# Kernel optimization log

Measured on AMD Instinct MI355X. Metric: run time of the kernel, lower is better.

## Reference

```python
import jax, jax.numpy as jnp
import numpy as np

B = 1; IMG = 256; P = 16; INC = 3; C = 384; NH = 12; HD = C // NH
WS = 8; SH = WS // 2; HP = IMG // P; L = HP * HP; NW = (HP // WS) ** 2
NB = 12; OC = 4; EPS = 1e-5; MLP = 4 * C


def _rel_index(w):
    coords = np.stack(np.meshgrid(np.arange(w), np.arange(w), indexing='ij'))
    cf = coords.reshape(2, -1)
    rel = (cf[:, :, None] - cf[:, None, :]).transpose(1, 2, 0)
    rel[:, :, 0] += w - 1
    rel[:, :, 1] += w - 1
    rel[:, :, 0] *= 2 * w - 1
    return rel.sum(-1)  # (w*w, w*w)


def _attn_mask():
    m = np.zeros((HP, HP))
    cnt = 0
    for hs in (slice(0, -WS), slice(-WS, -SH), slice(-SH, None)):
        for ws_ in (slice(0, -WS), slice(-WS, -SH), slice(-SH, None)):
            m[hs, ws_] = cnt
            cnt += 1
    mw = m.reshape(HP // WS, WS, HP // WS, WS).transpose(0, 2, 1, 3).reshape(-1, WS * WS)
    d = mw[:, None, :] - mw[:, :, None]
    return np.where(d != 0, -100.0, 0.0).astype(np.float32)  # (NW, 64, 64)

_REL_IDX = jnp.asarray(_rel_index(WS))
_AMASK = jnp.asarray(_attn_mask())


def _ln(x, w, b):
    m = jnp.mean(x, -1, keepdims=True)
    d = x - m
    v = jnp.mean(d * d, -1, keepdims=True)
    return d * jax.lax.rsqrt(v + EPS) * w + b


def _resize_ac(x, oh, ow):
    # bilinear, align_corners=True
    H, W = x.shape[-2], x.shape[-1]
    def idx(o, n):
        s = jnp.linspace(0.0, n - 1.0, o)
        i0 = jnp.floor(s).astype(jnp.int32)
        i1 = jnp.minimum(i0 + 1, n - 1)
        return i0, i1, (s - i0.astype(s.dtype)).astype(x.dtype)
    y0, y1, wy = idx(oh, H)
    x0, x1, wx = idx(ow, W)
    r = x[..., y0, :] * (1 - wy)[:, None] + x[..., y1, :] * wy[:, None]
    return r[..., x0] * (1 - wx) + r[..., x1] * wx


def setup_inputs():
    key = jax.random.key(0)
    ks = jax.random.split(key, 16)
    f32 = jnp.float32
    def rn(k, shape, s=0.02):
        return jax.random.normal(k, shape, dtype=f32) * s
    return {
        'x': jax.random.normal(ks[0], (B, INC, IMG, IMG), f32),
        'patch_w': rn(ks[1], (C, INC, P, P), 0.05),
        'patch_b': jnp.zeros((C,), f32),
        'pos_embed': rn(ks[2], (1, L, C)),
        'ln1_w': jnp.ones((NB, C), f32), 'ln1_b': jnp.zeros((NB, C), f32),
        'qkv_w': rn(ks[3], (NB, 3 * C, C)),
        'proj_w': rn(ks[4], (NB, C, C)), 'proj_b': jnp.zeros((NB, C), f32),
        'rpb': rn(ks[5], (NB, (2 * WS - 1) ** 2, NH)),
        'ln2_w': jnp.ones((NB, C), f32), 'ln2_b': jnp.zeros((NB, C), f32),
        'fc1_w': rn(ks[6], (NB, MLP, C)), 'fc1_b': jnp.zeros((NB, MLP), f32),
        'fc2_w': rn(ks[7], (NB, C, MLP)), 'fc2_b': jnp.zeros((NB, C), f32),
        'skip_w': rn(ks[8], (OC, C), 0.05), 'skip_b': jnp.zeros((OC,), f32),
        'dt1_w': rn(ks[9], (C, INC, P, P), 0.05), 'dt1_b': jnp.zeros((INC,), f32),
        'bn1_w': jnp.ones((INC,), f32), 'bn1_b': jnp.zeros((INC,), f32),
        'dt2_w': rn(ks[10], (INC, OC, P, P), 0.05), 'dt2_b': jnp.zeros((OC,), f32),
        'bn2_w': jnp.ones((OC,), f32), 'bn2_b': jnp.zeros((OC,), f32),
    }


def reference(x, patch_w, patch_b, pos_embed, ln1_w, ln1_b, qkv_w, proj_w, proj_b,
              rpb, ln2_w, ln2_b, fc1_w, fc1_b, fc2_w, fc2_b, skip_w, skip_b,
              dt1_w, dt1_b, bn1_w, bn1_b, dt2_w, dt2_b, bn2_w, bn2_b):
    scale = HD ** -0.5
    # --- patch embed (conv k=P, s=P) ---
    xr = x.reshape(B, INC, HP, P, HP, P)
    f = jnp.einsum('bchpwq,ocpq->bohw', xr, patch_w) + patch_b[None, :, None, None]
    # --- buggy token flatten, replicated exactly from the source ---
    t = jnp.transpose(f.reshape(B, C, P, HP // P, P, HP // P), (0, 3, 5, 1, 2, 4)).reshape(B, L, C)
    t = t + pos_embed

    def block(h, p):
        l1w, l1b, qw, pw, pb, rt, l2w, l2b, f1w, f1b, f2w, f2b = p
        sc = h
        y = _ln(h, l1w, l1b).reshape(B, HP, HP, C)
        y = jnp.roll(y, (-SH, -SH), axis=(1, 2))  # every block is shifted in this model
        yw = y.reshape(B, HP // WS, WS, HP // WS, WS, C).transpose(0, 1, 3, 2, 4, 5)
        yw = yw.reshape(B * NW, WS * WS, C)
        qkv = (yw @ qw.T).reshape(B * NW, WS * WS, 3, NH, HD).transpose(2, 0, 3, 1, 4)
        q, k, v = qkv[0], qkv[1], qkv[2]
        attn = jnp.einsum('wnid,wnjd->wnij', q, k) * scale
        bias = rt[_REL_IDX].transpose(2, 0, 1)  # (NH, 64, 64)
        attn = attn + bias[None]
        attn = attn.reshape(B, NW, NH, WS * WS, WS * WS) + _AMASK[None, :, None]
        attn = jax.nn.softmax(attn.reshape(B * NW, NH, WS * WS, WS * WS), axis=-1)
        o = jnp.einsum('wnij,wnjd->wnid', attn, v).transpose(0, 2, 1, 3).reshape(B * NW, WS * WS, C)
        o = o @ pw.T + pb
        o = o.reshape(B, HP // WS, HP // WS, WS, WS, C).transpose(0, 1, 3, 2, 4, 5).reshape(B, HP, HP, C)
        o = jnp.roll(o, (SH, SH), axis=(1, 2)).reshape(B, L, C)
        h = sc + o
        z = _ln(h, l2w, l2b)
        z = jax.nn.gelu(z @ f1w.T + f1b, approximate=False)
        h = h + (z @ f2w.T + f2b)
        return h, None

    t, _ = jax.lax.scan(block, t, (ln1_w, ln1_b, qkv_w, proj_w, proj_b, rpb,
                                   ln2_w, ln2_b, fc1_w, fc1_b, fc2_w, fc2_b))

    f = t.reshape(B, HP, HP, C).transpose(0, 3, 1, 2)  # (B, C, 16, 16)
    # --- decoder ---
    skip = jnp.einsum('bchw,oc->bohw', f, skip_w) + skip_b[None, :, None, None]
    # interpolate(skip, size=(H, W)) with H, W == skip's own size: identity.
    d = jnp.einsum('bchw,cokl->bohkwl', f, dt1_w).reshape(B, INC, HP * P, HP * P) + dt1_b[None, :, None, None]
    d = jax.nn.relu(d / jnp.sqrt(1.0 + EPS) * bn1_w[None, :, None, None] + bn1_b[None, :, None, None])
    d = jnp.einsum('bchw,cokl->bohkwl', d, dt2_w).reshape(B, OC, HP * P * P, HP * P * P) + dt2_b[None, :, None, None]
    d = d / jnp.sqrt(1.0 + EPS) * bn2_w[None, :, None, None] + bn2_b[None, :, None, None]
    # Upsample(scale_factor = IMG // (P*P) = 1): identity.
    skip_up = _resize_ac(skip, d.shape[2], d.shape[3])
    out = (d + skip_up).reshape(B, -1, IMG, IMG)
    return out
```

## Files before the change

kernel.cpp:

```cpp
#include <hip/hip_runtime.h>
#include <cmath>

typedef _Float16 v8h __attribute__((ext_vector_type(8)));
typedef float v4f __attribute__((ext_vector_type(4)));

#define DEV __device__ __forceinline__

DEV int win_map(int m) {
  int w = m >> 6, tok = m & 63;
  int r = ((w >> 1) * 8 + (tok >> 3) + 4) & 15;
  int c = ((w & 1) * 8 + (tok & 7) + 4) & 15;
  return r * 16 + c;
}

template<int MAP>
DEV float4 loadA4(const float* __restrict__ A, int m, int k, int K) {
  if constexpr (MAP == 0) {
    return *(const float4*)(A + (size_t)m * K + k);
  } else if constexpr (MAP == 1) {
    return *(const float4*)(A + (size_t)win_map(m) * 384 + k);
  } else {
    int h = m >> 4, w = m & 15;
    int inc = k >> 8, rem = k & 255, p = rem >> 4, q = rem & 15;
    return *(const float4*)(A + inc * 65536 + (h * 16 + p) * 256 + w * 16 + q);
  }
}

template<int WAVES_M, int WAVES_N, int WN, int MAP, bool LN, int EPI>
__launch_bounds__(256)
__global__ void mgemm(const float* __restrict__ A, const float* __restrict__ W,
                      const float* __restrict__ bias,
                      const float* __restrict__ lnw, const float* __restrict__ lnb,
                      const float* __restrict__ resid, const float* __restrict__ aux,
                      float* __restrict__ Cout, int N, int K) {
  constexpr int BM = WAVES_M * 16;
  constexpr int BN = WAVES_N * WN * 16;
  constexpr int BK = 64;
  constexpr int BKP = BK + 8;

  __shared__ _Float16 As[BM][BKP];
  __shared__ _Float16 Ws[BN][BKP];
  __shared__ float redS[256], redQ[256];
  __shared__ float lmean[BM], lrstd[BM];

  const int t = threadIdx.x;
  const int wave = t >> 6, lane = t & 63;
  const int m0 = blockIdx.y * BM, n0 = blockIdx.x * BN;

  if constexpr (LN) {
    constexpr int PARTS = 256 / BM;
    int r = t / PARTS, part = t % PARTS;
    int chunk = K / PARTS;
    float s = 0.f, sq = 0.f;
    for (int k = part * chunk; k < (part + 1) * chunk; k += 4) {
      float4 v = loadA4<MAP>(A, m0 + r, k, K);
      s += v.x + v.y + v.z + v.w;
      sq += v.x * v.x + v.y * v.y + v.z * v.z + v.w * v.w;
    }
    redS[t] = s; redQ[t] = sq;
    __syncthreads();
    if (t < BM) {
      float ss = 0.f, qq = 0.f;
      for (int p = 0; p < PARTS; ++p) { ss += redS[t * PARTS + p]; qq += redQ[t * PARTS + p]; }
      float mean = ss / K;
      float var = qq / K - mean * mean;
      lmean[t] = mean;
      lrstd[t] = rsqrtf(var + 1e-5f);
    }
    __syncthreads();
  }

  const int wm = wave % WAVES_M;
  const int wn = wave / WAVES_M;
  const int mBase = wm * 16;
  const int nBase = wn * (WN * 16);

  v4f acc[WN] = {};

  for (int k0 = 0; k0 < K; k0 += BK) {
    constexpr int AREP = (BM * 16) / 256;
#pragma unroll
    for (int i = 0; i < AREP; ++i) {
      int idx = t + i * 256;
      int row = idx >> 4;
      int kc = (idx & 15) * 4;
      float4 v = loadA4<MAP>(A, m0 + row, k0 + kc, K);
      if constexpr (LN) {
        float4 lw = *(const float4*)(lnw + k0 + kc);
        float4 lb = *(const float4*)(lnb + k0 + kc);
        float mu = lmean[row], rs = lrstd[row];
        v.x = (v.x - mu) * rs * lw.x + lb.x;
        v.y = (v.y - mu) * rs * lw.y + lb.y;
        v.z = (v.z - mu) * rs * lw.z + lb.z;
        v.w = (v.w - mu) * rs * lw.w + lb.w;
      }
      _Float16* dst = &As[row][kc];
      dst[0] = (_Float16)v.x; dst[1] = (_Float16)v.y;
      dst[2] = (_Float16)v.z; dst[3] = (_Float16)v.w;
    }
    constexpr int WREP = (BN * 16) / 256;
#pragma unroll
    for (int i = 0; i < WREP; ++i) {
      int idx = t + i * 256;
      int row = idx >> 4;
      int kc = (idx & 15) * 4;
      float4 v = *(const float4*)(W + (size_t)(n0 + row) * K + k0 + kc);
      _Float16* dst = &Ws[row][kc];
      dst[0] = (_Float16)v.x; dst[1] = (_Float16)v.y;
      dst[2] = (_Float16)v.z; dst[3] = (_Float16)v.w;
    }
    __syncthreads();
#pragma unroll
    for (int kk = 0; kk < BK; kk += 32) {
      v8h af = *(const v8h*)&As[mBase + (lane & 15)][kk + (lane >> 4) * 8];
#pragma unroll
      for (int nt = 0; nt < WN; ++nt) {
        v8h bf = *(const v8h*)&Ws[nBase + nt * 16 + (lane & 15)][kk + (lane >> 4) * 8];
        acc[nt] = __builtin_amdgcn_mfma_f32_16x16x32_f16(af, bf, acc[nt], 0, 0, 0);
      }
    }
    __syncthreads();
  }

  const int quad = lane >> 4;
  const int col = lane & 15;
#pragma unroll
  for (int nt = 0; nt < WN; ++nt) {
    int n = n0 + nBase + nt * 16 + col;
#pragma unroll
    for (int r = 0; r < 4; ++r) {
      int m = m0 + mBase + quad * 4 + r;
      float v = acc[nt][r];
      if constexpr (EPI == 0) {
        Cout[(size_t)m * N + n] = v;
      } else if constexpr (EPI == 1) {
        Cout[(size_t)m * N + n] = resid[(size_t)m * N + n] + v + bias[n];
      } else if constexpr (EPI == 2) {
        float z = v + bias[n];
        Cout[(size_t)m * N + n] = 0.5f * z * (1.0f + erff(z * 0.70710678118654752f));
      } else {
        Cout[n * 256 + m] = v + bias[n] + aux[n * 256 + m];
      }
    }
  }
}

__launch_bounds__(256)
__global__ void attn_k(const float* __restrict__ qkv, const float* __restrict__ rpb,
                       float* __restrict__ obuf) {
  __shared__ float qs[64][33], ks[64][33], vs[64][33];
  __shared__ float ps[64][68];
  __shared__ float rbias[225];
  __shared__ int labv[64];
  const int t = threadIdx.x;
  const int w = blockIdx.x & 3, head = blockIdx.x >> 2;

  for (int idx = t; idx < 2048; idx += 256) {
    int tok = idx >> 5, d = idx & 31;
    int base = (w * 64 + tok) * 1152 + head * 32 + d;
    qs[tok][d] = qkv[base];
    ks[tok][d] = qkv[base + 384];
    vs[tok][d] = qkv[base + 768];
  }
  for (int idx = t; idx < 225; idx += 256) rbias[idx] = rpb[idx * 12 + head];
  if (t < 64) {
    int r = (w >> 1) * 8 + (t >> 3), c = (w & 1) * 8 + (t & 7);
    int lr = r < 8 ? 0 : (r < 12 ? 1 : 2);
    int lc = c < 8 ? 0 : (c < 12 ? 1 : 2);
    labv[t] = lr * 3 + lc;
  }
  __syncthreads();

  const int tx = t & 15, ty = t >> 4;
  float acc[4][4] = {};
  for (int d = 0; d < 32; ++d) {
    float a[4], b[4];
#pragma unroll
    for (int ii = 0; ii < 4; ++ii) a[ii] = qs[ty * 4 + ii][d];
#pragma unroll
    for (int jj = 0; jj < 4; ++jj) b[jj] = ks[tx * 4 + jj][d];
#pragma unroll
    for (int ii = 0; ii < 4; ++ii)
#pragma unroll
      for (int jj = 0; jj < 4; ++jj) acc[ii][jj] += a[ii] * b[jj];
  }
  const float scale = 0.17677669529663687f;
#pragma unroll
  for (int ii = 0; ii < 4; ++ii) {
    int i = ty * 4 + ii;
    int yi = i >> 3, xi = i & 7, li = labv[i];
    float pv[4];
    float mx = -1e30f;
#pragma unroll
    for (int jj = 0; jj < 4; ++jj) {
      int j = tx * 4 + jj;
      int yj = j >> 3, xj = j & 7;
      int ri = (yi - yj + 7) * 15 + (xi - xj + 7);
      float s = acc[ii][jj] * scale + rbias[ri] + (li == labv[j] ? 0.f : -100.f);
      pv[jj] = s;
      mx = fmaxf(mx, s);
    }
    for (int off = 1; off < 16; off <<= 1) mx = fmaxf(mx, __shfl_xor(mx, off));
    float sum = 0.f;
#pragma unroll
    for (int jj = 0; jj < 4; ++jj) { pv[jj] = expf(pv[jj] - mx); sum += pv[jj]; }
    for (int off = 1; off < 16; off <<= 1) sum += __shfl_xor(sum, off);
    float inv = 1.0f / sum;
#pragma unroll
    for (int jj = 0; jj < 4; ++jj) ps[i][tx * 4 + jj] = pv[jj] * inv;
  }
  __syncthreads();

  float o2[4][2] = {};
  for (int j = 0; j < 64; ++j) {
    float v0 = vs[j][tx * 2 + 0], v1 = vs[j][tx * 2 + 1];
#pragma unroll
    for (int ii = 0; ii < 4; ++ii) {
      float p = ps[ty * 4 + ii][j];
      o2[ii][0] += p * v0;
      o2[ii][1] += p * v1;
    }
  }
#pragma unroll
  for (int ii = 0; ii < 4; ++ii) {
    int l = win_map(w * 64 + ty * 4 + ii);
    obuf[l * 384 + head * 32 + tx * 2 + 0] = o2[ii][0];
    obuf[l * 384 + head * 32 + tx * 2 + 1] = o2[ii][1];
  }
}

__global__ void skip_k(const float* __restrict__ hfin, const float* __restrict__ sw,
                       const float* __restrict__ sb, float* __restrict__ skipb) {
  int o = blockIdx.x, t = threadIdx.x;
  float acc = 0.f;
  for (int c = 0; c < 384; ++c) acc += hfin[t * 384 + c] * sw[o * 384 + c];
  skipb[o * 256 + t] = acc + sb[o];
}

__global__ void d1_k(const float* __restrict__ hfin, const float* __restrict__ wgt,
                     const float* __restrict__ bvec, const float* __restrict__ bnw,
                     const float* __restrict__ bnb, float* __restrict__ d1) {
  __shared__ float hs[2][384];
  const int t = threadIdx.x;
  const int l0 = blockIdx.x * 2;
  for (int idx = t; idx < 768; idx += 256) {
    int pi = idx / 384, c = idx % 384;
    hs[pi][c] = hfin[(l0 + pi) * 384 + c];
  }
  __syncthreads();
  const float invs = rsqrtf(1.0f + 1e-5f);
  const int kk = t >> 4, ll = t & 15;
  for (int o = 0; o < 3; ++o) {
    float a0 = 0.f, a1 = 0.f;
    for (int c = 0; c < 384; ++c) {
      float wv = wgt[c * 768 + o * 256 + t];
      a0 += hs[0][c] * wv;
      a1 += hs[1][c] * wv;
    }
    float sw = bnw[o] * invs, bb = bvec[o], sb = bnb[o];
    float v0 = fmaxf((a0 + bb) * sw + sb, 0.f);
    float v1 = fmaxf((a1 + bb) * sw + sb, 0.f);
#pragma unroll
    for (int pi = 0; pi < 2; ++pi) {
      int l = l0 + pi;
      int h = l >> 4, wq = l & 15;
      float v = pi ? v1 : v0;
      d1[o * 65536 + (h * 16 + kk) * 256 + (wq * 16 + ll)] = v;
    }
  }
}

__launch_bounds__(256)
__global__ void d2_k(const float* __restrict__ d1, const float* __restrict__ w2,
                     const float* __restrict__ b2, const float* __restrict__ bnw,
                     const float* __restrict__ bnb, const float* __restrict__ skipb,
                     float* __restrict__ out) {
  __shared__ float d1s[3][256];
  __shared__ float wcol[3][16];
  __shared__ float srow[16];
  const int t = threadIdx.x;
  const int y = blockIdx.x, o = blockIdx.y;
  const int h2 = y >> 4, k = y & 15;
  for (int idx = t; idx < 768; idx += 256) {
    int c = idx >> 8, wi = idx & 255;
    d1s[c][wi] = d1[c * 65536 + h2 * 256 + wi];
  }
  if (t < 48) {
    int c = t >> 4, l2 = t & 15;
    wcol[c][l2] = w2[c * 1024 + o * 256 + k * 16 + l2];
  }
  if (t < 16) {
    const float dy = 15.0f / 4095.0f;
    float s = y * dy;
    int y0 = min((int)s, 15);
    int y1 = min(y0 + 1, 15);
    float wy = s - (float)y0;
    float a0 = skipb[o * 256 + y0 * 16 + t];
    float a1 = skipb[o * 256 + y1 * 16 + t];
    srow[t] = a0 + (a1 - a0) * wy;
  }
  __syncthreads();
  const float invs = rsqrtf(1.0f + 1e-5f);
  const float sw = bnw[o] * invs;
  const float base = b2[o] * sw + bnb[o];
  const float dx = 15.0f / 4095.0f;
  const size_t obase = ((size_t)o << 24) + ((size_t)y << 12);
#pragma unroll
  for (int rep = 0; rep < 4; ++rep) {
    int x4 = t + rep * 256;
    int x = x4 * 4;
    int wi = x >> 4;
    int l2b = x & 15;
    float vals[4];
#pragma unroll
    for (int e = 0; e < 4; ++e) {
      int l2 = l2b + e;
      float v = d1s[0][wi] * wcol[0][l2] + d1s[1][wi] * wcol[1][l2] + d1s[2][wi] * wcol[2][l2];
      v = v * sw + base;
      float s = (float)(x + e) * dx;
      int x0 = min((int)s, 15);
      int x1 = min(x0 + 1, 15);
      float wx = s - (float)x0;
      vals[e] = v + srow[x0] + (srow[x1] - srow[x0]) * wx;
    }
    *(float4*)&out[obase + x] = make_float4(vals[0], vals[1], vals[2], vals[3]);
  }
}

extern "C" void kernel_launch(void* const* d_in, const int* in_sizes, int n_in,
                              void* d_out, int out_size, void* d_ws, size_t ws_size,
                              hipStream_t stream) {
  const float* x       = (const float*)d_in[0];
  const float* patch_w = (const float*)d_in[1];
  const float* patch_b = (const float*)d_in[2];
  const float* pos     = (const float*)d_in[3];
  const float* ln1w    = (const float*)d_in[4];
  const float* ln1b    = (const float*)d_in[5];
  const float* qkvw    = (const float*)d_in[6];
  const float* projw   = (const float*)d_in[7];
  const float* projb   = (const float*)d_in[8];
  const float* rpb     = (const float*)d_in[9];
  const float* ln2w    = (const float*)d_in[10];
  const float* ln2b    = (const float*)d_in[11];
  const float* fc1w    = (const float*)d_in[12];
  const float* fc1b    = (const float*)d_in[13];
  const float* fc2w    = (const float*)d_in[14];
  const float* fc2b    = (const float*)d_in[15];
  const float* skipw   = (const float*)d_in[16];
  const float* skipbi  = (const float*)d_in[17];
  const float* dt1w    = (const float*)d_in[18];
  const float* dt1b    = (const float*)d_in[19];
  const float* bn1w    = (const float*)d_in[20];
  const float* bn1b    = (const float*)d_in[21];
  const float* dt2w    = (const float*)d_in[22];
  const float* dt2b    = (const float*)d_in[23];
  const float* bn2w    = (const float*)d_in[24];
  const float* bn2b    = (const float*)d_in[25];
  float* out = (float*)d_out;
  float* ws = (float*)d_ws;

  float* h    = ws;
  float* qkvb = ws + 98304;
  float* obuf = ws + 393216;
  float* zb   = ws + 491520;
  float* d1b  = ws + 884736;
  float* skb  = ws + 1081344;

  mgemm<2, 2, 2, 2, false, 3><<<dim3(6, 8), 256, 0, stream>>>(
      x, patch_w, patch_b, nullptr, nullptr, nullptr, pos, h, 384, 768);

  for (int b = 0; b < 12; ++b) {
    mgemm<2, 2, 2, 1, true, 0><<<dim3(18, 8), 256, 0, stream>>>(
        h, qkvw + (size_t)b * 442368, nullptr, ln1w + b * 384, ln1b + b * 384,
        nullptr, nullptr, qkvb, 1152, 384);
    attn_k<<<48, 256, 0, stream>>>(qkvb, rpb + b * 2700, obuf);
    mgemm<1, 4, 1, 0, false, 1><<<dim3(6, 16), 256, 0, stream>>>(
        obuf, projw + (size_t)b * 147456, projb + b * 384, nullptr, nullptr,
        h, nullptr, h, 384, 384);
    mgemm<2, 2, 2, 0, true, 2><<<dim3(24, 8), 256, 0, stream>>>(
        h, fc1w + (size_t)b * 589824, fc1b + b * 1536, ln2w + b * 384, ln2b + b * 384,
        nullptr, nullptr, zb, 1536, 384);
    mgemm<1, 4, 1, 0, false, 1><<<dim3(6, 16), 256, 0, stream>>>(
        zb, fc2w + (size_t)b * 589824, fc2b + b * 384, nullptr, nullptr,
        h, nullptr, h, 384, 1536);
  }

  skip_k<<<4, 256, 0, stream>>>(h, skipw, skipbi, skb);
  d1_k<<<128, 256, 0, stream>>>(h, dt1w, dt1b, bn1w, bn1b, d1b);
  d2_k<<<dim3(4096, 4), 256, 0, stream>>>(d1b, dt2w, dt2b, bn2w, bn2b, skb, out);
}
```

Baseline: 1.408 ms.

## Fuse encoder launches into persistent megakernel with software grid barriers

```diff
diff --git a/kernel.cpp b/kernel.cpp
--- a/kernel.cpp
+++ b/kernel.cpp
@@ -5,6 +5,8 @@
 typedef float v4f __attribute__((ext_vector_type(4)));
 
 #define DEV __device__ __forceinline__
+
+constexpr int GRID = 256;
 
 DEV int win_map(int m) {
   int w = m >> 6, tok = m & 63;
@@ -26,26 +28,48 @@
   }
 }
 
+union SMem {
+  struct {
+    _Float16 As[32][72];
+    _Float16 Ws[64][72];
+    float redS[256], redQ[256];
+    float lmean[32], lrstd[32];
+  } g;
+  struct {
+    float qs[64][33], ks[64][33], vs[64][33];
+    float ps[64][68];
+    float rbias[225];
+    int lab[64];
+  } a;
+  struct {
+    float hs[2][384];
+  } d;
+};
+
+DEV void gsync(unsigned* cnt, unsigned& bar, int t) {
+  __threadfence();
+  __syncthreads();
+  bar += GRID;
+  if (t == 0) {
+    __hip_atomic_fetch_add(cnt, 1u, __ATOMIC_RELEASE, __HIP_MEMORY_SCOPE_AGENT);
+    while (__hip_atomic_load(cnt, __ATOMIC_RELAXED, __HIP_MEMORY_SCOPE_AGENT) < bar)
+      __builtin_amdgcn_s_sleep(1);
+    (void)__hip_atomic_load(cnt, __ATOMIC_ACQUIRE, __HIP_MEMORY_SCOPE_AGENT);
+  }
+  __syncthreads();
+}
+
 template<int WAVES_M, int WAVES_N, int WN, int MAP, bool LN, int EPI>
-__launch_bounds__(256)
-__global__ void mgemm(const float* __restrict__ A, const float* __restrict__ W,
-                      const float* __restrict__ bias,
-                      const float* __restrict__ lnw, const float* __restrict__ lnb,
-                      const float* __restrict__ resid, const float* __restrict__ aux,
-                      float* __restrict__ Cout, int N, int K) {
+DEV void gemm_tile(SMem& sm, const int t, const int m0, const int n0,
+                   const float* __restrict__ A, const float* __restrict__ W,
+                   const float* __restrict__ bias,
+                   const float* __restrict__ lnw, const float* __restrict__ lnb,
+                   const float* __restrict__ resid, const float* __restrict__ aux,
+                   float* __restrict__ Cout, int N, int K) {
   constexpr int BM = WAVES_M * 16;
   constexpr int BN = WAVES_N * WN * 16;
   constexpr int BK = 64;
-  constexpr int BKP = BK + 8;
-
-  __shared__ _Float16 As[BM][BKP];
-  __shared__ _Float16 Ws[BN][BKP];
-  __shared__ float redS[256], redQ[256];
-  __shared__ float lmean[BM], lrstd[BM];
-
-  const int t = threadIdx.x;
   const int wave = t >> 6, lane = t & 63;
-  const int m0 = blockIdx.y * BM, n0 = blockIdx.x * BN;
 
   if constexpr (LN) {
     constexpr int PARTS = 256 / BM;
@@ -57,15 +81,15 @@
       s += v.x + v.y + v.z + v.w;
       sq += v.x * v.x + v.y * v.y + v.z * v.z + v.w * v.w;
     }
-    redS[t] = s; redQ[t] = sq;
+    sm.g.redS[t] = s; sm.g.redQ[t] = sq;
     __syncthreads();
     if (t < BM) {
       float ss = 0.f, qq = 0.f;
-      for (int p = 0; p < PARTS; ++p) { ss += redS[t * PARTS + p]; qq += redQ[t * PARTS + p]; }
+      for (int p = 0; p < PARTS; ++p) { ss += sm.g.redS[t * PARTS + p]; qq += sm.g.redQ[t * PARTS + p]; }
       float mean = ss / K;
       float var = qq / K - mean * mean;
-      lmean[t] = mean;
-      lrstd[t] = rsqrtf(var + 1e-5f);
+      sm.g.lmean[t] = mean;
+      sm.g.lrstd[t] = rsqrtf(var + 1e-5f);
     }
     __syncthreads();
   }
@@ -88,13 +112,13 @@
       if constexpr (LN) {
         float4 lw = *(const float4*)(lnw + k0 + kc);
         float4 lb = *(const float4*)(lnb + k0 + kc);
-        float mu = lmean[row], rs = lrstd[row];
+        float mu = sm.g.lmean[row], rs = sm.g.lrstd[row];
         v.x = (v.x - mu) * rs * lw.x + lb.x;
         v.y = (v.y - mu) * rs * lw.y + lb.y;
         v.z = (v.z - mu) * rs * lw.z + lb.z;
         v.w = (v.w - mu) * rs * lw.w + lb.w;
       }
-      _Float16* dst = &As[row][kc];
+      _Float16* dst = &sm.g.As[row][kc];
       dst[0] = (_Float16)v.x; dst[1] = (_Float16)v.y;
       dst[2] = (_Float16)v.z; dst[3] = (_Float16)v.w;
     }
@@ -105,17 +129,17 @@
       int row = idx >> 4;
       int kc = (idx & 15) * 4;
       float4 v = *(const float4*)(W + (size_t)(n0 + row) * K + k0 + kc);
-      _Float16* dst = &Ws[row][kc];
+      _Float16* dst = &sm.g.Ws[row][kc];
       dst[0] = (_Float16)v.x; dst[1] = (_Float16)v.y;
       dst[2] = (_Float16)v.z; dst[3] = (_Float16)v.w;
     }
     __syncthreads();
 #pragma unroll
     for (int kk = 0; kk < BK; kk += 32) {
-      v8h af = *(const v8h*)&As[mBase + (lane & 15)][kk + (lane >> 4) * 8];
+      v8h af = *(const v8h*)&sm.g.As[mBase + (lane & 15)][kk + (lane >> 4) * 8];
 #pragma unroll
       for (int nt = 0; nt < WN; ++nt) {
-        v8h bf = *(const v8h*)&Ws[nBase + nt * 16 + (lane & 15)][kk + (lane >> 4) * 8];
+        v8h bf = *(const v8h*)&sm.g.Ws[nBase + nt * 16 + (lane & 15)][kk + (lane >> 4) * 8];
         acc[nt] = __builtin_amdgcn_mfma_f32_16x16x32_f16(af, bf, acc[nt], 0, 0, 0);
       }
     }
@@ -145,29 +169,24 @@
   }
 }
 
-__launch_bounds__(256)
-__global__ void attn_k(const float* __restrict__ qkv, const float* __restrict__ rpb,
-                       float* __restrict__ obuf) {
-  __shared__ float qs[64][33], ks[64][33], vs[64][33];
-  __shared__ float ps[64][68];
-  __shared__ float rbias[225];
-  __shared__ int labv[64];
-  const int t = threadIdx.x;
-  const int w = blockIdx.x & 3, head = blockIdx.x >> 2;
+DEV void attn_tile(SMem& sm, const int t, const int bid,
+                   const float* __restrict__ qkv, const float* __restrict__ rpb,
+                   float* __restrict__ obuf) {
+  const int w = bid & 3, head = bid >> 2;
 
   for (int idx = t; idx < 2048; idx += 256) {
     int tok = idx >> 5, d = idx & 31;
     int base = (w * 64 + tok) * 1152 + head * 32 + d;
-    qs[tok][d] = qkv[base];
-    ks[tok][d] = qkv[base + 384];
-    vs[tok][d] = qkv[base + 768];
-  }
-  for (int idx = t; idx < 225; idx += 256) rbias[idx] = rpb[idx * 12 + head];
+    sm.a.qs[tok][d] = qkv[base];
+    sm.a.ks[tok][d] = qkv[base + 384];
+    sm.a.vs[tok][d] = qkv[base + 768];
+  }
+  for (int idx = t; idx < 225; idx += 256) sm.a.rbias[idx] = rpb[idx * 12 + head];
   if (t < 64) {
     int r = (w >> 1) * 8 + (t >> 3), c = (w & 1) * 8 + (t & 7);
     int lr = r < 8 ? 0 : (r < 12 ? 1 : 2);
     int lc = c < 8 ? 0 : (c < 12 ? 1 : 2);
-    labv[t] = lr * 3 + lc;
+    sm.a.lab[t] = lr * 3 + lc;
   }
   __syncthreads();
 
@@ -176,9 +195,9 @@
   for (int d = 0; d < 32; ++d) {
     float a[4], b[4];
 #pragma unroll
-    for (int ii = 0; ii < 4; ++ii) a[ii] = qs[ty * 4 + ii][d];
-#pragma unroll
-    for (int jj = 0; jj < 4; ++jj) b[jj] = ks[tx * 4 + jj][d];
+    for (int ii = 0; ii < 4; ++ii) a[ii] = sm.a.qs[ty * 4 + ii][d];
+#pragma unroll
+    for (int jj = 0; jj < 4; ++jj) b[jj] = sm.a.ks[tx * 4 + jj][d];
 #pragma unroll
     for (int ii = 0; ii < 4; ++ii)
 #pragma unroll
@@ -188,7 +207,7 @@
 #pragma unroll
   for (int ii = 0; ii < 4; ++ii) {
     int i = ty * 4 + ii;
-    int yi = i >> 3, xi = i & 7, li = labv[i];
+    int yi = i >> 3, xi = i & 7, li = sm.a.lab[i];
     float pv[4];
     float mx = -1e30f;
 #pragma unroll
@@ -196,7 +215,7 @@
       int j = tx * 4 + jj;
       int yj = j >> 3, xj = j & 7;
       int ri = (yi - yj + 7) * 15 + (xi - xj + 7);
-      float s = acc[ii][jj] * scale + rbias[ri] + (li == labv[j] ? 0.f : -100.f);
+      float s = acc[ii][jj] * scale + sm.a.rbias[ri] + (li == sm.a.lab[j] ? 0.f : -100.f);
       pv[jj] = s;
       mx = fmaxf(mx, s);
     }
@@ -207,16 +226,16 @@
     for (int off = 1; off < 16; off <<= 1) sum += __shfl_xor(sum, off);
     float inv = 1.0f / sum;
 #pragma unroll
-    for (int jj = 0; jj < 4; ++jj) ps[i][tx * 4 + jj] = pv[jj] * inv;
+    for (int jj = 0; jj < 4; ++jj) sm.a.ps[i][tx * 4 + jj] = pv[jj] * inv;
   }
   __syncthreads();
 
   float o2[4][2] = {};
   for (int j = 0; j < 64; ++j) {
-    float v0 = vs[j][tx * 2 + 0], v1 = vs[j][tx * 2 + 1];
+    float v0 = sm.a.vs[j][tx * 2 + 0], v1 = sm.a.vs[j][tx * 2 + 1];
 #pragma unroll
     for (int ii = 0; ii < 4; ++ii) {
-      float p = ps[ty * 4 + ii][j];
+      float p = sm.a.ps[ty * 4 + ii][j];
       o2[ii][0] += p * v0;
       o2[ii][1] += p * v1;
     }
@@ -229,23 +248,14 @@
   }
 }
 
-__global__ void skip_k(const float* __restrict__ hfin, const float* __restrict__ sw,
-                       const float* __restrict__ sb, float* __restrict__ skipb) {
-  int o = blockIdx.x, t = threadIdx.x;
-  float acc = 0.f;
-  for (int c = 0; c < 384; ++c) acc += hfin[t * 384 + c] * sw[o * 384 + c];
-  skipb[o * 256 + t] = acc + sb[o];
-}
-
-__global__ void d1_k(const float* __restrict__ hfin, const float* __restrict__ wgt,
-                     const float* __restrict__ bvec, const float* __restrict__ bnw,
-                     const float* __restrict__ bnb, float* __restrict__ d1) {
-  __shared__ float hs[2][384];
-  const int t = threadIdx.x;
-  const int l0 = blockIdx.x * 2;
+DEV void d1_tile(SMem& sm, const int t, const int bid,
+                 const float* __restrict__ hfin, const float* __restrict__ wgt,
+                 const float* __restrict__ bvec, const float* __restrict__ bnw,
+                 const float* __restrict__ bnb, float* __restrict__ d1) {
+  const int l0 = bid * 2;
   for (int idx = t; idx < 768; idx += 256) {
     int pi = idx / 384, c = idx % 384;
-    hs[pi][c] = hfin[(l0 + pi) * 384 + c];
+    sm.d.hs[pi][c] = hfin[(l0 + pi) * 384 + c];
   }
   __syncthreads();
   const float invs = rsqrtf(1.0f + 1e-5f);
@@ -254,8 +264,8 @@
     float a0 = 0.f, a1 = 0.f;
     for (int c = 0; c < 384; ++c) {
       float wv = wgt[c * 768 + o * 256 + t];
-      a0 += hs[0][c] * wv;
-      a1 += hs[1][c] * wv;
+      a0 += sm.d.hs[0][c] * wv;
+      a1 += sm.d.hs[1][c] * wv;
     }
     float sw = bnw[o] * invs, bb = bvec[o], sb = bnb[o];
     float v0 = fmaxf((a0 + bb) * sw + sb, 0.f);
@@ -268,6 +278,78 @@
       d1[o * 65536 + (h * 16 + kk) * 256 + (wq * 16 + ll)] = v;
     }
   }
+}
+
+DEV void skip_tile(const int t, const int o,
+                   const float* __restrict__ hfin, const float* __restrict__ sw,
+                   const float* __restrict__ sb, float* __restrict__ skipb) {
+  float acc = 0.f;
+  for (int c = 0; c < 384; ++c) acc += hfin[t * 384 + c] * sw[o * 384 + c];
+  skipb[o * 256 + t] = acc + sb[o];
+}
+
+struct Params {
+  const float *x, *patch_w, *patch_b, *pos;
+  const float *ln1w, *ln1b, *qkvw, *projw, *projb, *rpb, *ln2w, *ln2b;
+  const float *fc1w, *fc1b, *fc2w, *fc2b;
+  const float *skipw, *skipbi, *dt1w, *dt1b, *bn1w, *bn1b;
+  float *h, *qkvb, *obuf, *zb, *d1b, *skb;
+  unsigned* cnt;
+};
+
+__launch_bounds__(256)
+__global__ void mega_k(Params p) {
+  __shared__ SMem sm;
+  const int t = threadIdx.x;
+  const int bid = blockIdx.x;
+  unsigned bar = 0;
+
+  if (bid < 48) {
+    gemm_tile<2, 2, 2, 2, false, 3>(sm, t, (bid / 6) * 32, (bid % 6) * 64,
+        p.x, p.patch_w, p.patch_b, nullptr, nullptr, nullptr, p.pos, p.h, 384, 768);
+  }
+  gsync(p.cnt, bar, t);
+
+  for (int b = 0; b < 12; ++b) {
+    const float* qw  = p.qkvw + (size_t)b * 442368;
+    const float* pw  = p.projw + (size_t)b * 147456;
+    const float* pb  = p.projb + b * 384;
+    const float* f1w = p.fc1w + (size_t)b * 589824;
+    const float* f1b = p.fc1b + b * 1536;
+    const float* f2w = p.fc2w + (size_t)b * 589824;
+    const float* f2b = p.fc2b + b * 384;
+
+    if (bid < 144)
+      gemm_tile<2, 2, 2, 1, true, 0>(sm, t, (bid / 18) * 32, (bid % 18) * 64,
+          p.h, qw, nullptr, p.ln1w + b * 384, p.ln1b + b * 384,
+          nullptr, nullptr, p.qkvb, 1152, 384);
+    gsync(p.cnt, bar, t);
+
+    if (bid < 48)
+      attn_tile(sm, t, bid, p.qkvb, p.rpb + b * 2700, p.obuf);
+    gsync(p.cnt, bar, t);
+
+    if (bid < 96)
+      gemm_tile<1, 4, 1, 0, false, 1>(sm, t, (bid / 6) * 16, (bid % 6) * 64,
+          p.obuf, pw, pb, nullptr, nullptr, p.h, nullptr, p.h, 384, 384);
+    gsync(p.cnt, bar, t);
+
+    if (bid < 192)
+      gemm_tile<2, 2, 2, 0, true, 2>(sm, t, (bid / 24) * 32, (bid % 24) * 64,
+          p.h, f1w, f1b, p.ln2w + b * 384, p.ln2b + b * 384,
+          nullptr, nullptr, p.zb, 1536, 384);
+    gsync(p.cnt, bar, t);
+
+    if (bid < 96)
+      gemm_tile<1, 4, 1, 0, false, 1>(sm, t, (bid / 6) * 16, (bid % 6) * 64,
+          p.zb, f2w, f2b, nullptr, nullptr, p.h, nullptr, p.h, 384, 1536);
+    gsync(p.cnt, bar, t);
+  }
+
+  if (bid < 128)
+    d1_tile(sm, t, bid, p.h, p.dt1w, p.dt1b, p.bn1w, p.bn1b, p.d1b);
+  else if (bid < 132)
+    skip_tile(t, bid - 128, p.h, p.skipw, p.skipbi, p.skb);
 }
 
 __launch_bounds__(256)
@@ -330,62 +412,46 @@
 extern "C" void kernel_launch(void* const* d_in, const int* in_sizes, int n_in,
                               void* d_out, int out_size, void* d_ws, size_t ws_size,
                               hipStream_t stream) {
-  const float* x       = (const float*)d_in[0];
-  const float* patch_w = (const float*)d_in[1];
-  const float* patch_b = (const float*)d_in[2];
-  const float* pos     = (const float*)d_in[3];
-  const float* ln1w    = (const float*)d_in[4];
-  const float* ln1b    = (const float*)d_in[5];
-  const float* qkvw    = (const float*)d_in[6];
-  const float* projw   = (const float*)d_in[7];
-  const float* projb   = (const float*)d_in[8];
-  const float* rpb     = (const float*)d_in[9];
-  const float* ln2w    = (const float*)d_in[10];
-  const float* ln2b    = (const float*)d_in[11];
-  const float* fc1w    = (const float*)d_in[12];
-  const float* fc1b    = (const float*)d_in[13];
-  const float* fc2w    = (const float*)d_in[14];
-  const float* fc2b    = (const float*)d_in[15];
-  const float* skipw   = (const float*)d_in[16];
-  const float* skipbi  = (const float*)d_in[17];
-  const float* dt1w    = (const float*)d_in[18];
-  const float* dt1b    = (const float*)d_in[19];
-  const float* bn1w    = (const float*)d_in[20];
-  const float* bn1b    = (const float*)d_in[21];
-  const float* dt2w    = (const float*)d_in[22];
-  const float* dt2b    = (const float*)d_in[23];
-  const float* bn2w    = (const float*)d_in[24];
-  const float* bn2b    = (const float*)d_in[25];
+  Params p;
+  p.x       = (const float*)d_in[0];
+  p.patch_w = (const float*)d_in[1];
+  p.patch_b = (const float*)d_in[2];
+  p.pos     = (const float*)d_in[3];
+  p.ln1w    = (const float*)d_in[4];
+  p.ln1b    = (const float*)d_in[5];
+  p.qkvw    = (const float*)d_in[6];
+  p.projw   = (const float*)d_in[7];
+  p.projb   = (const float*)d_in[8];
+  p.rpb     = (const float*)d_in[9];
+  p.ln2w    = (const float*)d_in[10];
+  p.ln2b    = (const float*)d_in[11];
+  p.fc1w    = (const float*)d_in[12];
+  p.fc1b    = (const float*)d_in[13];
+  p.fc2w    = (const float*)d_in[14];
+  p.fc2b    = (const float*)d_in[15];
+  p.skipw   = (const float*)d_in[16];
+  p.skipbi  = (const float*)d_in[17];
+  p.dt1w    = (const float*)d_in[18];
+  p.dt1b    = (const float*)d_in[19];
+  p.bn1w    = (const float*)d_in[20];
+  p.bn1b    = (const float*)d_in[21];
+  const float* dt2w = (const float*)d_in[22];
+  const float* dt2b = (const float*)d_in[23];
+  const float* bn2w = (const float*)d_in[24];
+  const float* bn2b = (const float*)d_in[25];
   float* out = (float*)d_out;
-  float* ws = (float*)d_ws;
-
-  float* h    = ws;
-  float* qkvb = ws + 98304;
-  float* obuf = ws + 393216;
-  float* zb   = ws + 491520;
-  float* d1b  = ws + 884736;
-  float* skb  = ws + 1081344;
-
-  mgemm<2, 2, 2, 2, false, 3><<<dim3(6, 8), 256, 0, stream>>>(
-      x, patch_w, patch_b, nullptr, nullptr, nullptr, pos, h, 384, 768);
-
-  for (int b = 0; b < 12; ++b) {
-    mgemm<2, 2, 2, 1, true, 0><<<dim3(18, 8), 256, 0, stream>>>(
-        h, qkvw + (size_t)b * 442368, nullptr, ln1w + b * 384, ln1b + b * 384,
-        nullptr, nullptr, qkvb, 1152, 384);
-    attn_k<<<48, 256, 0, stream>>>(qkvb, rpb + b * 2700, obuf);
-    mgemm<1, 4, 1, 0, false, 1><<<dim3(6, 16), 256, 0, stream>>>(
-        obuf, projw + (size_t)b * 147456, projb + b * 384, nullptr, nullptr,
-        h, nullptr, h, 384, 384);
-    mgemm<2, 2, 2, 0, true, 2><<<dim3(24, 8), 256, 0, stream>>>(
-        h, fc1w + (size_t)b * 589824, fc1b + b * 1536, ln2w + b * 384, ln2b + b * 384,
-        nullptr, nullptr, zb, 1536, 384);
-    mgemm<1, 4, 1, 0, false, 1><<<dim3(6, 16), 256, 0, stream>>>(
-        zb, fc2w + (size_t)b * 589824, fc2b + b * 384, nullptr, nullptr,
-        h, nullptr, h, 384, 1536);
-  }
-
-  skip_k<<<4, 256, 0, stream>>>(h, skipw, skipbi, skb);
-  d1_k<<<128, 256, 0, stream>>>(h, dt1w, dt1b, bn1w, bn1b, d1b);
-  d2_k<<<dim3(4096, 4), 256, 0, stream>>>(d1b, dt2w, dt2b, bn2w, bn2b, skb, out);
-}
+
+  p.cnt = (unsigned*)d_ws;
+  float* base = (float*)((char*)d_ws + 256);
+  p.h    = base;
+  p.qkvb = base + 98304;
+  p.obuf = base + 393216;
+  p.zb   = base + 491520;
+  p.d1b  = base + 884736;
+  p.skb  = base + 1081344;
+
+  hipMemsetAsync(d_ws, 0, 256, stream);
+
+  mega_k<<<GRID, 256, 0, stream>>>(p);
+  d2_k<<<dim3(4096, 4), 256, 0, stream>>>(p.d1b, dt2w, dt2b, bn2w, bn2b, p.skb, out);
+}
```

After: 3.148 ms. 124% more time.
